# Kernel tuning notes

Measured on AMD Instinct MI355X. Metric: run time of the kernel, lower is better.

Reference implementation:

```python
import jax, jax.numpy as jnp
import numpy as np

INPUT_DIM, ENC_H, DEC_H, HORIZON = 8, 384, 384, 18
B, L = 1024, 336


def _lstm_layer(xs, Wih, Whh, bih, bhh):
    # xs: [B, L, D] -> outputs [B, L, H], final h [B, H]
    Bv = xs.shape[0]
    Hh = Whh.shape[1]
    def step(carry, x_t):
        h, c = carry
        z = x_t @ Wih.T + h @ Whh.T + bih + bhh  # [B, 4H], gate order i,f,g,o (PyTorch)
        i, f, g, o = jnp.split(z, 4, axis=-1)
        c = jax.nn.sigmoid(f) * c + jax.nn.sigmoid(i) * jnp.tanh(g)
        h = jax.nn.sigmoid(o) * jnp.tanh(c)
        return (h, c), h
    init = (jnp.zeros((Bv, Hh), xs.dtype), jnp.zeros((Bv, Hh), xs.dtype))
    (h, c), ys = jax.lax.scan(step, init, jnp.swapaxes(xs, 0, 1))
    return jnp.swapaxes(ys, 0, 1), h


def setup_inputs() -> dict:
    key = jax.random.key(0)
    ks = jax.random.split(key, 20)
    s = 0.05
    d = {
        "x": jax.random.normal(ks[0], (B, L, INPUT_DIM), jnp.float32),
        "future_feats": jax.random.normal(ks[1], (B, HORIZON, 4), jnp.float32),
        # encoder layer 0
        "enc_Wih0": jax.random.normal(ks[2], (4 * ENC_H, INPUT_DIM), jnp.float32) * s,
        "enc_Whh0": jax.random.normal(ks[3], (4 * ENC_H, ENC_H), jnp.float32) * s,
        "enc_bih0": jax.random.normal(ks[4], (4 * ENC_H,), jnp.float32) * s,
        "enc_bhh0": jax.random.normal(ks[5], (4 * ENC_H,), jnp.float32) * s,
        # encoder layer 1
        "enc_Wih1": jax.random.normal(ks[6], (4 * ENC_H, ENC_H), jnp.float32) * s,
        "enc_Whh1": jax.random.normal(ks[7], (4 * ENC_H, ENC_H), jnp.float32) * s,
        "enc_bih1": jax.random.normal(ks[8], (4 * ENC_H,), jnp.float32) * s,
        "enc_bhh1": jax.random.normal(ks[9], (4 * ENC_H,), jnp.float32) * s,
        # attention projection (no bias)
        "Wa": jax.random.normal(ks[10], (DEC_H, ENC_H), jnp.float32) * s,
        # dec_in: Linear(1+4+enc_h -> dec_h)
        "dec_in_W": jax.random.normal(ks[11], (DEC_H, 1 + 4 + ENC_H), jnp.float32) * s,
        "dec_in_b": jax.random.normal(ks[12], (DEC_H,), jnp.float32) * s,
        # decoder LSTM (1 layer)
        "dec_Wih": jax.random.normal(ks[13], (4 * DEC_H, DEC_H), jnp.float32) * s,
        "dec_Whh": jax.random.normal(ks[14], (4 * DEC_H, DEC_H), jnp.float32) * s,
        "dec_bih": jax.random.normal(ks[15], (4 * DEC_H,), jnp.float32) * s,
        "dec_bhh": jax.random.normal(ks[16], (4 * DEC_H,), jnp.float32) * s,
        # output head
        "out_W": jax.random.normal(ks[17], (1, DEC_H), jnp.float32) * s,
        "out_b": jax.random.normal(ks[18], (1,), jnp.float32) * s,
    }
    return d


def reference(x, future_feats, enc_Wih0, enc_Whh0, enc_bih0, enc_bhh0,
              enc_Wih1, enc_Whh1, enc_bih1, enc_bhh1, Wa, dec_in_W, dec_in_b,
              dec_Wih, dec_Whh, dec_bih, dec_bhh, out_W, out_b):
    Bv = x.shape[0]
    # 2-layer encoder (eval mode: inter-layer dropout inactive)
    h1, _ = _lstm_layer(x, enc_Wih0, enc_Whh0, enc_bih0, enc_bhh0)
    enc_out, h_last = _lstm_layer(h1, enc_Wih1, enc_Whh1, enc_bih1, enc_bhh1)
    proj = enc_out @ Wa.T  # [B, L, dec_h] (Wa(enc_out) is step-invariant)

    def dec_step(carry, feat_t):
        h, c, y_prev = carry
        scores = jnp.einsum('bld,bd->bl', proj, h)
        alpha = jax.nn.softmax(scores, axis=1)
        ctx = jnp.einsum('bl,bld->bd', alpha, enc_out)
        din = jnp.concatenate([y_prev, feat_t, ctx], axis=1)  # [B, 1+4+enc_h]
        din = jax.nn.relu(din @ dec_in_W.T + dec_in_b)
        z = din @ dec_Wih.T + h @ dec_Whh.T + dec_bih + dec_bhh
        i, f, g, o = jnp.split(z, 4, axis=-1)
        c = jax.nn.sigmoid(f) * c + jax.nn.sigmoid(i) * jnp.tanh(g)
        h = jax.nn.sigmoid(o) * jnp.tanh(c)
        y_t = h @ out_W.T + out_b  # [B, 1]
        y_prev = jax.lax.stop_gradient(y_t)  # .detach() in torch
        return (h, c, y_prev), y_t

    init = (h_last, jnp.zeros_like(h_last), jnp.zeros((Bv, 1), x.dtype))
    _, ys = jax.lax.scan(dec_step, init, jnp.swapaxes(future_feats, 0, 1))
    return jnp.swapaxes(ys, 0, 1)  # [B, horizon, 1]
```

## Files before the change

### kernel.cpp

```cpp
#include <hip/hip_runtime.h>
#include <stdint.h>

typedef __bf16 bf16;
typedef __bf16 bf16x8 __attribute__((ext_vector_type(8)));
typedef short  s16x8  __attribute__((ext_vector_type(8)));
typedef float  f32x4  __attribute__((ext_vector_type(4)));
typedef uint32_t u32;

#define NB   1024
#define LSEQ 336
#define HID  384
#define HOR  18
#define SMEM_BYTES 36864

__device__ bf16  g_H0[(size_t)(LSEQ+1)*NB*HID];
__device__ bf16  g_enc[(size_t)NB*LSEQ*HID];
__device__ bf16  g_zero[HID];
__device__ bf16  g_Adec[2*NB*768];
__device__ bf16  g_Adin[NB*416];
__device__ bf16  g_xb[NB*LSEQ*8];
__device__ float g_c0[NB*HID];
__device__ float g_c1[NB*HID];
__device__ float g_cdec[NB*HID];
__device__ float g_u[NB*HID];
__device__ float g_bias0[1536], g_bias1[1536], g_biasd[1536], g_biasdin[384];
__device__ bf16  g_Bp0[12*13*4096];
__device__ bf16  g_Bp1n[24*24*4*64*8];
__device__ bf16  g_Bpd[12*24*4096];
__device__ bf16  g_Bpi[3*13*4096];
__device__ bf16  g_Bpu[3*12*4096];
__device__ int   g_f0[8*LSEQ];
__device__ int   g_f1[4*(LSEQ+1)];

__device__ __forceinline__ float sigf(float x){ return 1.0f/(1.0f + __expf(-x)); }
__device__ __forceinline__ float tanh_f(float x){
  x = fminf(fmaxf(x, -15.f), 15.f);
  float e = __expf(2.f*x);
  return (e - 1.f)/(e + 1.f);
}

__device__ __forceinline__ void ds16(bf16* p, s16x8 v){
  union{ s16x8 v; uint64_t q[2]; } u; u.v = v;
  __hip_atomic_store((uint64_t*)p,     u.q[0], __ATOMIC_RELAXED, __HIP_MEMORY_SCOPE_AGENT);
  __hip_atomic_store((uint64_t*)p + 1, u.q[1], __ATOMIC_RELAXED, __HIP_MEMORY_SCOPE_AGENT);
}

__global__ void zero_state_k(){
  int i = blockIdx.x*blockDim.x + threadIdx.x;
  int st = gridDim.x*blockDim.x;
  bf16 z = (bf16)0.f;
  for(int k=i;k<NB*HID;k+=st){ g_H0[k]=z; g_c0[k]=0.f; g_c1[k]=0.f; g_cdec[k]=0.f; }
  for(int k=i;k<8*LSEQ;k+=st) g_f0[k]=0;
  for(int k=i;k<4*(LSEQ+1);k+=st) g_f1[k]=0;
}

__global__ void pack_xb_k(const float* __restrict__ x){
  int i = blockIdx.x*256 + threadIdx.x;
  int n = NB*LSEQ*8;
  for(int k=i; k<n; k+=gridDim.x*256) g_xb[k] = (bf16)x[k];
}

__global__ void pack_gates_k(int mode, const float* __restrict__ W1, const float* __restrict__ W2,
                             int nks){
  bf16* out = (mode==0)? g_Bp0 : g_Bpd;
  size_t idx = (size_t)blockIdx.x*256 + threadIdx.x;
  size_t total = (size_t)12*nks*512;
  if(idx >= total) return;
  int lane = (int)(idx & 63);
  int tt   = (int)((idx>>6) & 7);
  size_t tmp = idx >> 9;
  int ks = (int)(tmp % nks);
  int jb = (int)(tmp / nks);
  int n  = (tt>>1)*HID + jb*32 + (tt&1)*16 + (lane&15);
  int kb = ks*32 + (lane>>4)*8;
  bf16x8 v;
  #pragma unroll
  for(int i=0;i<8;i++){
    int k = kb + i;
    float f;
    if(mode==0) f = (k<384) ? W1[(size_t)n*384 + k] : (k<392 ? W2[(size_t)n*8 + (k-384)] : 0.f);
    else        f = (k<384) ? W1[(size_t)n*384 + k] : W2[(size_t)n*384 + (k-384)];
    v[i] = (bf16)f;
  }
  *(bf16x8*)(out + idx*8) = v;
}

__global__ void pack_gates16_k(const float* __restrict__ Wih1, const float* __restrict__ Whh1){
  int idx = blockIdx.x*256 + threadIdx.x;
  if(idx >= 24*24*4*64) return;
  int lane = idx&63, rem = idx>>6;
  int g = rem&3; rem >>= 2;
  int ks = rem%24, jn = rem/24;
  int n  = g*HID + jn*16 + (lane&15);
  int kb = ks*32 + (lane>>4)*8;
  bf16x8 v;
  #pragma unroll
  for(int i=0;i<8;i++){
    int k = kb+i;
    float f = (k<384)? Wih1[(size_t)n*384 + k] : Whh1[(size_t)n*384 + (k-384)];
    v[i] = (bf16)f;
  }
  *(bf16x8*)(g_Bp1n + (size_t)idx*8) = v;
}

__global__ void pack_plain_k(int mode, const float* __restrict__ W, int nks, int nb_cnt){
  bf16* out = mode ? g_Bpu : g_Bpi;
  size_t idx = (size_t)blockIdx.x*256 + threadIdx.x;
  size_t total = (size_t)nb_cnt*nks*512;
  if(idx>=total) return;
  int lane = (int)(idx&63);
  int tt   = (int)((idx>>6)&7);
  size_t tmp = idx>>9;
  int ks = (int)(tmp%nks);
  int nb = (int)(tmp/nks);
  int n  = nb*128 + tt*16 + (lane&15);
  int kb = ks*32 + (lane>>4)*8;
  bf16x8 v;
  #pragma unroll
  for(int i=0;i<8;i++){
    int k = kb+i;
    float f;
    if(mode==0) f = (k<389)? W[(size_t)n*389 + k] : 0.f;
    else        f = W[(size_t)k*384 + n];
    v[i]=(bf16)f;
  }
  *(bf16x8*)(out + idx*8) = v;
}

__global__ void prep_misc_k(const float* bih0,const float* bhh0,const float* bih1,const float* bhh1,
                            const float* dbih,const float* dbhh,const float* dinb){
  int i = blockIdx.x*256 + threadIdx.x;
  if(i<1536){ g_bias0[i]=bih0[i]+bhh0[i]; g_bias1[i]=bih1[i]+bhh1[i]; g_biasd[i]=dbih[i]+dbhh[i]; }
  if(i<384) g_biasdin[i]=dinb[i];
}

__device__ __forceinline__ void spin_ge(int* p, int tgt){
  while(__hip_atomic_load(p, __ATOMIC_RELAXED, __HIP_MEMORY_SCOPE_AGENT) < tgt)
    __builtin_amdgcn_s_sleep(1);
}

__global__ __launch_bounds__(256,1)
void enc6_k(){
  extern __shared__ char lds[];
  const int bid = blockIdx.x, tid = threadIdx.x;
  const int lane = tid&63, wv = tid>>6;
  const int l15 = lane&15, lk = (lane>>4)*8;

  if(bid < 96){
    const int g = bid & 7, jb = bid >> 3;
    { const s16x8* src = (const s16x8*)(g_Bp0 + (size_t)jb*13*4096);
      s16x8* dst = (s16x8*)lds;
      #pragma unroll
      for(int h=0;h<26;h++) dst[tid + h*256] = src[tid + h*256];
    }
    bf16* tr = (bf16*)(lds + 13*8192);
    __syncthreads();
    const int jj0 = jb*32 + l15;
    float bia[2],bfa[2],bga[2],boa[2];
    #pragma unroll
    for(int jh=0;jh<2;jh++){
      bia[jh]=g_bias0[jj0+jh*16];     bfa[jh]=g_bias0[384+jj0+jh*16];
      bga[jh]=g_bias0[768+jj0+jh*16]; boa[jh]=g_bias0[1152+jj0+jh*16];
    }
    size_t hoff[2], xoff[2];
    #pragma unroll
    for(int mt=0;mt<2;mt++){
      int row = g*128 + wv*32 + mt*16 + l15;
      hoff[mt] = (size_t)row*HID + lk;
      xoff[mt] = (size_t)row*LSEQ*8;
    }
    float c[2][2][4] = {};
    for(int w=0; w<LSEQ; w++){
      if(tid==0 && w>=1) spin_ge(&g_f0[g*LSEQ + (w-1)], 12);
      __syncthreads();
      asm volatile("" ::: "memory");
      const bf16* H0w = g_H0 + (size_t)w*NB*HID;
      bf16x8 af[13][2];
      #pragma unroll
      for(int ks=0;ks<12;ks++)
        #pragma unroll
        for(int mt=0;mt<2;mt++)
          af[ks][mt] = *(const bf16x8*)(H0w + hoff[mt] + ks*32);
      #pragma unroll
      for(int mt=0;mt<2;mt++){
        bf16x8 z;
        #pragma unroll
        for(int e=0;e<8;e++) z[e]=(bf16)0.f;
        if(lk==0) z = *(const bf16x8*)(g_xb + xoff[mt] + (size_t)w*8);
        af[12][mt] = z;
      }
      f32x4 acc[2][8];
      #pragma unroll
      for(int m2=0;m2<2;m2++)
        #pragma unroll
        for(int tt=0;tt<8;tt++) acc[m2][tt] = (f32x4){0.f,0.f,0.f,0.f};
      #pragma unroll
      for(int ks=0;ks<13;ks++){
        #pragma unroll
        for(int tt=0;tt<8;tt++){
          bf16x8 bfr = *(const bf16x8*)(lds + (ks*8+tt)*1024 + lane*16);
          acc[0][tt] = __builtin_amdgcn_mfma_f32_16x16x32_bf16(af[ks][0], bfr, acc[0][tt],0,0,0);
          acc[1][tt] = __builtin_amdgcn_mfma_f32_16x16x32_bf16(af[ks][1], bfr, acc[1][tt],0,0,0);
        }
      }
      #pragma unroll
      for(int mt=0;mt<2;mt++)
        #pragma unroll
        for(int jh=0;jh<2;jh++)
          #pragma unroll
          for(int r=0;r<4;r++){
            float zi=acc[mt][0+jh][r]+bia[jh], zf=acc[mt][2+jh][r]+bfa[jh],
                  zg=acc[mt][4+jh][r]+bga[jh], zo=acc[mt][6+jh][r]+boa[jh];
            size_t ci = (size_t)(g*128 + wv*32 + mt*16 + (lane>>4)*4 + r)*HID + jj0 + jh*16;
            float cn = sigf(zf)*g_c0[ci] + sigf(zi)*tanh_f(zg);
            g_c0[ci] = cn;
            int lr = wv*32 + mt*16 + (lane>>4)*4 + r;
            tr[lr*32 + jh*16 + l15] = (bf16)(sigf(zo)*tanh_f(cn));
          }
      __syncthreads();
      bf16* H0n = g_H0 + (size_t)(w+1)*NB*HID;
      #pragma unroll
      for(int h=0;h<2;h++){
        int p = tid + h*256;
        int row = p>>2, cc = p&3;
        s16x8 v = *(const s16x8*)(tr + row*32 + cc*8);
        ds16(H0n + (size_t)(g*128+row)*HID + jb*32 + cc*8, v);
      }
      __syncthreads();
      if(tid==0)
        __hip_atomic_fetch_add(&g_f0[g*LSEQ + w], 1, __ATOMIC_RELAXED, __HIP_MEMORY_SCOPE_AGENT);
    }
  } else {
    const int idx = bid-96, m = idx & 3, jn = idx >> 2;
    { const s16x8* src = (const s16x8*)(g_Bp1n + (size_t)jn*24*2048);
      s16x8* dst = (s16x8*)lds;
      #pragma unroll
      for(int h=0;h<24;h++) dst[tid + h*256] = src[tid + h*256];
    }
    bf16* tr = (bf16*)(lds + 24*4096);
    __syncthreads();
    const int jj = jn*16 + l15;
    const float bi=g_bias1[jj], bff=g_bias1[384+jj], bg=g_bias1[768+jj], bo=g_bias1[1152+jj];
    int rows[4]; size_t hoff[4];
    #pragma unroll
    for(int mt=0;mt<4;mt++){
      rows[mt] = m*256 + wv*64 + mt*16 + l15;
      hoff[mt] = (size_t)rows[mt]*HID + lk;
    }
    float c[4][4] = {};
    for(int s=1; s<=LSEQ; s++){
      if(tid==0){
        spin_ge(&g_f0[(2*m)*LSEQ + (s-1)], 12);
        spin_ge(&g_f0[(2*m+1)*LSEQ + (s-1)], 12);
        if(s>=2) spin_ge(&g_f1[m*(LSEQ+1) + (s-1)], 24);
      }
      __syncthreads();
      asm volatile("" ::: "memory");
      const bf16* H0s = g_H0 + (size_t)s*NB*HID;
      const size_t strideE = (s>=2)? (size_t)LSEQ*HID : 0;
      const bf16* Es = (s>=2)? (g_enc + (size_t)(s-2)*HID) : g_zero;
      size_t eoff[4];
      #pragma unroll
      for(int mt=0;mt<4;mt++) eoff[mt] = (size_t)rows[mt]*strideE + lk;
      bf16x8 ap[8][4];
      #pragma unroll
      for(int d=0; d<8; d++)
        #pragma unroll
        for(int mt=0;mt<4;mt++)
          ap[d][mt] = *(const bf16x8*)(H0s + hoff[mt] + d*32);
      f32x4 acc[4][4];
      #pragma unroll
      for(int mt=0;mt<4;mt++)
        #pragma unroll
        for(int g4=0;g4<4;g4++) acc[mt][g4] = (f32x4){0.f,0.f,0.f,0.f};
      #pragma unroll
      for(int ks=0;ks<24;ks++){
        bf16x8 bfr[4];
        #pragma unroll
        for(int g4=0;g4<4;g4++) bfr[g4] = *(const bf16x8*)(lds + (ks*4+g4)*1024 + lane*16);
        bf16x8 a[4];
        #pragma unroll
        for(int mt=0;mt<4;mt++) a[mt] = ap[ks&7][mt];
        int kn = ks+8;
        if(kn<24){
          if(kn<12){
            #pragma unroll
            for(int mt=0;mt<4;mt++) ap[ks&7][mt] = *(const bf16x8*)(H0s + hoff[mt] + kn*32);
          } else {
            #pragma unroll
            for(int mt=0;mt<4;mt++) ap[ks&7][mt] = *(const bf16x8*)(Es + eoff[mt] + (kn-12)*32);
          }
        }
        #pragma unroll
        for(int mt=0;mt<4;mt++)
          #pragma unroll
          for(int g4=0;g4<4;g4++)
            acc[mt][g4] = __builtin_amdgcn_mfma_f32_16x16x32_bf16(a[mt], bfr[g4], acc[mt][g4],0,0,0);
      }
      #pragma unroll
      for(int mt=0;mt<4;mt++)
        #pragma unroll
        for(int r=0;r<4;r++){
          float zi=acc[mt][0][r]+bi, zf=acc[mt][1][r]+bff,
                zg=acc[mt][2][r]+bg, zo=acc[mt][3][r]+bo;
          size_t ci = (size_t)(m*256 + wv*64 + mt*16 + (lane>>4)*4 + r)*HID + jj;
          float cn = sigf(zf)*g_c1[ci] + sigf(zi)*tanh_f(zg);
          g_c1[ci] = cn;
          int lr = wv*64 + mt*16 + (lane>>4)*4 + r;
          tr[lr*16 + l15] = (bf16)(sigf(zo)*tanh_f(cn));
        }
      __syncthreads();
      const int t = s-1;
      #pragma unroll
      for(int h=0;h<2;h++){
        int p = tid + h*256;
        int row = p>>1, hf2 = p&1;
        s16x8 v = *(const s16x8*)(tr + row*16 + hf2*8);
        ds16(g_enc + ((size_t)(m*256+row)*LSEQ + t)*HID + jn*16 + hf2*8, v);
      }
      __syncthreads();
      if(tid==0)
        __hip_atomic_fetch_add(&g_f1[m*(LSEQ+1) + s], 1, __ATOMIC_RELAXED, __HIP_MEMORY_SCOPE_AGENT);
    }
  }
}

struct SReg { s16x8 a0,a1,b0,b1; };

__device__ __forceinline__ void stage_load(const bf16* __restrict__ A, int ldA,
                                           const bf16* __restrict__ Bk, int tid, SReg& sr){
  int c0 = tid, c1 = tid+256;
  sr.a0 = *(const s16x8*)(A + (size_t)(c0>>2)*ldA + (c0&3)*8);
  sr.a1 = *(const s16x8*)(A + (size_t)(c1>>2)*ldA + (c1&3)*8);
  const s16x8* B8 = (const s16x8*)Bk;
  sr.b0 = B8[c0]; sr.b1 = B8[c1];
}

__device__ __forceinline__ void stage_write(char* Ab, char* Bb, int tid, const SReg& sr){
  int c0 = tid, c1 = tid+256;
  *(s16x8*)(Ab + (c0>>2)*80 + (c0&3)*16) = sr.a0;
  *(s16x8*)(Ab + (c1>>2)*80 + (c1&3)*16) = sr.a1;
  *(s16x8*)(Bb + c0*16) = sr.b0;
  *(s16x8*)(Bb + c1*16) = sr.b1;
}

__device__ __forceinline__ void gemm_core(const bf16* __restrict__ A, int ldA,
                                          const bf16* __restrict__ Bp, int nks,
                                          char* smem, f32x4 acc[4][4]){
  const int tid = threadIdx.x;
  const int lane = tid & 63, wv = tid>>6, wm = wv>>1, wn = wv&1;
  char* Ab0 = smem;            char* Ab1 = smem + 10240;
  char* Bb0 = smem + 20480;    char* Bb1 = smem + 28672;
  f32x4 z = {0.f,0.f,0.f,0.f};
  #pragma unroll
  for(int m=0;m<4;m++)
    #pragma unroll
    for(int g=0;g<4;g++) acc[m][g]=z;
  SReg sr;
  stage_load(A, ldA, Bp, tid, sr);
  stage_write(Ab0, Bb0, tid, sr);
  const int aoff = (wm*64 + (lane&15))*80 + (lane>>4)*16;
  const int boff = wn*1024 + lane*16;
  for(int ks=0; ks<nks; ks++){
    char* Ac = (ks&1)? Ab1: Ab0;
    char* Bc = (ks&1)? Bb1: Bb0;
    char* An = (ks&1)? Ab0: Ab1;
    char* Bn = (ks&1)? Bb0: Bb1;
    bool more = (ks+1)<nks;
    if(more) stage_load(A + (ks+1)*32, ldA, Bp + (size_t)(ks+1)*4096, tid, sr);
    __syncthreads();
    bf16x8 af[4], bfr[4];
    #pragma unroll
    for(int mt=0;mt<4;mt++) af[mt] = *(const bf16x8*)(Ac + aoff + mt*16*80);
    #pragma unroll
    for(int g=0;g<4;g++)    bfr[g] = *(const bf16x8*)(Bc + boff + g*2048);
    #pragma unroll
    for(int mt=0;mt<4;mt++)
      #pragma unroll
      for(int g=0;g<4;g++)
        acc[mt][g] = __builtin_amdgcn_mfma_f32_16x16x32_bf16(af[mt], bfr[g], acc[mt][g], 0,0,0);
    if(more) stage_write(An, Bn, tid, sr);
  }
}

__device__ __forceinline__ void lstm_epi(f32x4 acc[4][4], int mbase, int jb,
     const float* __restrict__ bias, float* __restrict__ cst,
     bf16* __restrict__ d0, int ld0, bf16* __restrict__ d1, size_t ld1){
  int lane = threadIdx.x&63, wv = threadIdx.x>>6, wm = wv>>1, wn = wv&1;
  int j = jb*32 + wn*16 + (lane&15);
  float bi = bias[j], bff = bias[384+j], bg = bias[768+j], bo = bias[1152+j];
  #pragma unroll
  for(int mt=0;mt<4;mt++){
    #pragma unroll
    for(int r=0;r<4;r++){
      int brow = mbase + wm*64 + mt*16 + (lane>>4)*4 + r;
      float zi = acc[mt][0][r]+bi, zf = acc[mt][1][r]+bff,
            zg = acc[mt][2][r]+bg, zo = acc[mt][3][r]+bo;
      size_t ci = (size_t)brow*HID + j;
      float cold = cst[ci];
      float cn = sigf(zf)*cold + sigf(zi)*tanh_f(zg);
      cst[ci] = cn;
      bf16 hb = (bf16)(sigf(zo)*tanh_f(cn));
      d0[(size_t)brow*ld0 + j] = hb;
      if(d1) d1[(size_t)brow*ld1 + j] = hb;
    }
  }
}

__global__ __launch_bounds__(256)
void dec_lstm_k(int t){
  __shared__ char smem[SMEM_BYTES];
  int bid = blockIdx.x, mb = bid/12, jb = bid%12;
  int rs = t&1, wsl = rs^1;
  f32x4 acc[4][4];
  gemm_core(g_Adec + (size_t)rs*NB*768 + (size_t)mb*128*768, 768,
            g_Bpd + (size_t)jb*24*4096, 24, smem, acc);
  lstm_epi(acc, mb*128, jb, g_biasd, g_cdec,
           g_Adec + (size_t)wsl*NB*768 + 384, 768, (bf16*)nullptr, 0);
}

__global__ __launch_bounds__(256)
void plain_gemm_k(int t, int mode){
  __shared__ char smem[SMEM_BYTES];
  int bid = blockIdx.x, mb = bid/3, nb = bid%3;
  int rs = t&1;
  const bf16* A; int ldA, nks; const bf16* Bp;
  if(mode==1){ A = g_Adec + (size_t)rs*NB*768 + 384; ldA=768; Bp = g_Bpu; nks=12; }
  else       { A = g_Adin;                           ldA=416; Bp = g_Bpi; nks=13; }
  f32x4 acc[4][4];
  gemm_core(A + (size_t)mb*128*ldA, ldA, Bp + (size_t)nb*nks*4096, nks, smem, acc);
  int lane = threadIdx.x&63, wv = threadIdx.x>>6, wm = wv>>1, wn = wv&1;
  bf16* dbf = g_Adec + (size_t)rs*NB*768;
  #pragma unroll
  for(int mt=0;mt<4;mt++){
    #pragma unroll
    for(int ti=0;ti<4;ti++){
      int n = nb*128 + (ti*2+wn)*16 + (lane&15);
      #pragma unroll
      for(int r=0;r<4;r++){
        int brow = mb*128 + wm*64 + mt*16 + (lane>>4)*4 + r;
        float v = acc[mt][ti][r];
        if(mode==0){ v += g_biasdin[n]; v = fmaxf(v,0.f); dbf[(size_t)brow*768 + n] = (bf16)v; }
        else g_u[(size_t)brow*384 + n] = v;
      }
    }
  }
}

__global__ __launch_bounds__(256)
void attn_k(){
  __shared__ float sm[4][392];
  int tid = threadIdx.x, lane = tid&63, w = tid>>6;
  int bl = w>>1, hf = w&1;
  int b = blockIdx.x*2 + bl;
  const float* ub = g_u + (size_t)b*HID + lane*6;
  float u0=ub[0],u1=ub[1],u2=ub[2],u3=ub[3],u4=ub[4],u5=ub[5];
  const u32* er = (const u32*)(g_enc + (size_t)b*LSEQ*HID) + (size_t)hf*168*192 + lane*3;
  float m=-1e30f, den=0.f, a0=0,a1=0,a2=0,a3=0,a4=0,a5=0;
  for(int l=0;l<168;l++){
    u32 w0 = er[0], w1 = er[1], w2 = er[2];
    er += 192;
    float e0 = __uint_as_float(w0<<16);
    float e1 = __uint_as_float(w0 & 0xffff0000u);
    float e2 = __uint_as_float(w1<<16);
    float e3 = __uint_as_float(w1 & 0xffff0000u);
    float e4 = __uint_as_float(w2<<16);
    float e5 = __uint_as_float(w2 & 0xffff0000u);
    float p = e0*u0 + e1*u1 + e2*u2 + e3*u3 + e4*u4 + e5*u5;
    #pragma unroll
    for(int o=1;o<64;o<<=1) p += __shfl_xor(p, o, 64);
    float mn = fmaxf(m, p);
    float al = __expf(m - mn), pe = __expf(p - mn);
    den = den*al + pe;
    a0 = a0*al + pe*e0; a1 = a1*al + pe*e1; a2 = a2*al + pe*e2;
    a3 = a3*al + pe*e3; a4 = a4*al + pe*e4; a5 = a5*al + pe*e5;
    m = mn;
  }
  if(lane==0){ sm[w][0]=m; sm[w][1]=den; }
  sm[w][2+lane*6+0]=a0; sm[w][2+lane*6+1]=a1; sm[w][2+lane*6+2]=a2;
  sm[w][2+lane*6+3]=a3; sm[w][2+lane*6+4]=a4; sm[w][2+lane*6+5]=a5;
  __syncthreads();
  if(hf==0){
    float m2 = sm[w+1][0], d2 = sm[w+1][1];
    float M = fmaxf(m, m2);
    float f1 = __expf(m - M), f2 = __expf(m2 - M);
    float inv = 1.f/(den*f1 + d2*f2);
    bf16* cd = g_Adin + (size_t)b*416 + 5 + lane*6;
    cd[0] = (bf16)((a0*f1 + sm[w+1][2+lane*6+0]*f2)*inv);
    cd[1] = (bf16)((a1*f1 + sm[w+1][2+lane*6+1]*f2)*inv);
    cd[2] = (bf16)((a2*f1 + sm[w+1][2+lane*6+2]*f2)*inv);
    cd[3] = (bf16)((a3*f1 + sm[w+1][2+lane*6+3]*f2)*inv);
    cd[4] = (bf16)((a4*f1 + sm[w+1][2+lane*6+4]*f2)*inv);
    cd[5] = (bf16)((a5*f1 + sm[w+1][2+lane*6+5]*f2)*inv);
  }
}

__global__ void post_k(int t, const float* __restrict__ outW,
                       const float* __restrict__ outb, float* __restrict__ out,
                       const float* __restrict__ ff){
  int b = blockIdx.x*256 + threadIdx.x;
  if(b>=NB) return;
  int wsl = (t&1)^1;
  const s16x8* hp = (const s16x8*)(g_Adec + (size_t)wsl*NB*768 + (size_t)b*768 + 384);
  float acc = 0.f;
  #pragma unroll 4
  for(int i=0;i<48;i++){
    s16x8 v = hp[i];
    #pragma unroll
    for(int e=0;e<8;e++){
      float hv = __uint_as_float(((u32)(uint16_t)v[e])<<16);
      acc += hv*outW[i*8+e];
    }
  }
  float y = acc + outb[0];
  out[(size_t)b*HOR + t] = y;
  g_Adin[(size_t)b*416] = (bf16)y;
  if(t+1<HOR){
    #pragma unroll
    for(int k=0;k<4;k++) g_Adin[(size_t)b*416 + 1 + k] = (bf16)ff[(size_t)b*HOR*4 + (t+1)*4 + k];
  }
}

__global__ void dec_prep_k(const float* __restrict__ ff){
  int i = blockIdx.x*256 + threadIdx.x;
  if(i < NB*HID){
    int b = i/HID, j = i%HID;
    g_Adec[(size_t)b*768 + 384 + j] = g_enc[(size_t)b*LSEQ*HID + (size_t)(LSEQ-1)*HID + j];
  }
  if(i < NB*4){
    int b = i>>2, k = i&3;
    g_Adin[(size_t)b*416 + 1 + k] = (bf16)ff[(size_t)b*HOR*4 + k];
  }
  if(i < NB) g_Adin[(size_t)i*416] = (bf16)0.f;
}

extern "C" void kernel_launch(void* const* d_in, const int* in_sizes, int n_in,
                              void* d_out, int out_size, void* d_ws, size_t ws_size,
                              hipStream_t stream){
  const float* x    = (const float*)d_in[0];
  const float* ff   = (const float*)d_in[1];
  const float* Wih0 = (const float*)d_in[2];
  const float* Whh0 = (const float*)d_in[3];
  const float* bih0 = (const float*)d_in[4];
  const float* bhh0 = (const float*)d_in[5];
  const float* Wih1 = (const float*)d_in[6];
  const float* Whh1 = (const float*)d_in[7];
  const float* bih1 = (const float*)d_in[8];
  const float* bhh1 = (const float*)d_in[9];
  const float* Wa   = (const float*)d_in[10];
  const float* dinW = (const float*)d_in[11];
  const float* dinb = (const float*)d_in[12];
  const float* dWih = (const float*)d_in[13];
  const float* dWhh = (const float*)d_in[14];
  const float* dbih = (const float*)d_in[15];
  const float* dbhh = (const float*)d_in[16];
  const float* outW = (const float*)d_in[17];
  const float* outb = (const float*)d_in[18];
  float* out = (float*)d_out;

  zero_state_k<<<1024,256,0,stream>>>();
  pack_xb_k<<<2048,256,0,stream>>>(x);
  pack_gates_k<<<(12*13*512)/256,256,0,stream>>>(0, Whh0, Wih0, 13);
  pack_gates16_k<<<576,256,0,stream>>>(Wih1, Whh1);
  pack_gates_k<<<(12*24*512)/256,256,0,stream>>>(2, dWih, dWhh, 24);
  pack_plain_k<<<(3*13*512)/256,256,0,stream>>>(0, dinW, 13, 3);
  pack_plain_k<<<(3*12*512)/256,256,0,stream>>>(1, Wa, 12, 3);
  prep_misc_k<<<8,256,0,stream>>>(bih0,bhh0,bih1,bhh1,dbih,dbhh,dinb);

  hipFuncSetAttribute((const void*)enc6_k,
                      hipFuncAttributeMaxDynamicSharedMemorySize, 114688);
  enc6_k<<<192,256,114688,stream>>>();

  dec_prep_k<<<1536,256,0,stream>>>(ff);
  for(int t=0;t<HOR;t++){
    plain_gemm_k<<<24,256,0,stream>>>(t, 1);
    attn_k<<<512,256,0,stream>>>();
    plain_gemm_k<<<24,256,0,stream>>>(t, 0);
    dec_lstm_k<<<96,256,0,stream>>>(t);
    post_k<<<4,256,0,stream>>>(t, outW, outb, out, ff);
  }
  (void)in_sizes; (void)n_in; (void)out_size; (void)d_ws; (void)ws_size;
}
```

Measured before the change: 8.753 ms.

## Keep encoder cell state in registers and fold output projection into next GEMM

Both encoder LSTM layers now carry the cell state in per-thread registers instead of reading and writing g_c0/g_c1 in global memory every timestep. This removes that global traffic and the zeroing of those buffers. The layer-1 blocks now split their three flag spin-waits across three threads so the waits run concurrently. In the decoder, the output projection and the writes of y_prev and the next step's features move into the next step's first plain_gemm launch, leaving a single post_k launch after the loop and cutting one launch per decoder step. This relies on each thread always owning the same (row, column) cell elements across timesteps, and it adds some register pressure in the persistent encoder kernel.

```diff
diff --git a/kernel.cpp b/kernel.cpp
--- a/kernel.cpp
+++ b/kernel.cpp
@@ -19,8 +19,6 @@
 __device__ bf16  g_Adec[2*NB*768];
 __device__ bf16  g_Adin[NB*416];
 __device__ bf16  g_xb[NB*LSEQ*8];
-__device__ float g_c0[NB*HID];
-__device__ float g_c1[NB*HID];
 __device__ float g_cdec[NB*HID];
 __device__ float g_u[NB*HID];
 __device__ float g_bias0[1536], g_bias1[1536], g_biasd[1536], g_biasdin[384];
@@ -49,7 +47,7 @@
   int i = blockIdx.x*blockDim.x + threadIdx.x;
   int st = gridDim.x*blockDim.x;
   bf16 z = (bf16)0.f;
-  for(int k=i;k<NB*HID;k+=st){ g_H0[k]=z; g_c0[k]=0.f; g_c1[k]=0.f; g_cdec[k]=0.f; }
+  for(int k=i;k<NB*HID;k+=st){ g_H0[k]=z; g_cdec[k]=0.f; }
   for(int k=i;k<8*LSEQ;k+=st) g_f0[k]=0;
   for(int k=i;k<4*(LSEQ+1);k+=st) g_f1[k]=0;
 }
@@ -140,7 +138,7 @@
 }
 
 __global__ __launch_bounds__(256,1)
-void enc6_k(){
+void enc7_k(){
   extern __shared__ char lds[];
   const int bid = blockIdx.x, tid = threadIdx.x;
   const int lane = tid&63, wv = tid>>6;
@@ -211,9 +209,8 @@
           for(int r=0;r<4;r++){
             float zi=acc[mt][0+jh][r]+bia[jh], zf=acc[mt][2+jh][r]+bfa[jh],
                   zg=acc[mt][4+jh][r]+bga[jh], zo=acc[mt][6+jh][r]+boa[jh];
-            size_t ci = (size_t)(g*128 + wv*32 + mt*16 + (lane>>4)*4 + r)*HID + jj0 + jh*16;
-            float cn = sigf(zf)*g_c0[ci] + sigf(zi)*tanh_f(zg);
-            g_c0[ci] = cn;
+            float cn = sigf(zf)*c[mt][jh][r] + sigf(zi)*tanh_f(zg);
+            c[mt][jh][r]=cn;
             int lr = wv*32 + mt*16 + (lane>>4)*4 + r;
             tr[lr*32 + jh*16 + l15] = (bf16)(sigf(zo)*tanh_f(cn));
           }
@@ -249,11 +246,9 @@
     }
     float c[4][4] = {};
     for(int s=1; s<=LSEQ; s++){
-      if(tid==0){
-        spin_ge(&g_f0[(2*m)*LSEQ + (s-1)], 12);
-        spin_ge(&g_f0[(2*m+1)*LSEQ + (s-1)], 12);
-        if(s>=2) spin_ge(&g_f1[m*(LSEQ+1) + (s-1)], 24);
-      }
+      if(tid==0)           spin_ge(&g_f0[(2*m)*LSEQ + (s-1)], 12);
+      else if(tid==1)      spin_ge(&g_f0[(2*m+1)*LSEQ + (s-1)], 12);
+      else if(tid==2 && s>=2) spin_ge(&g_f1[m*(LSEQ+1) + (s-1)], 24);
       __syncthreads();
       asm volatile("" ::: "memory");
       const bf16* H0s = g_H0 + (size_t)s*NB*HID;
@@ -303,9 +298,8 @@
         for(int r=0;r<4;r++){
           float zi=acc[mt][0][r]+bi, zf=acc[mt][1][r]+bff,
                 zg=acc[mt][2][r]+bg, zo=acc[mt][3][r]+bo;
-          size_t ci = (size_t)(m*256 + wv*64 + mt*16 + (lane>>4)*4 + r)*HID + jj;
-          float cn = sigf(zf)*g_c1[ci] + sigf(zi)*tanh_f(zg);
-          g_c1[ci] = cn;
+          float cn = sigf(zf)*c[mt][r] + sigf(zi)*tanh_f(zg);
+          c[mt][r]=cn;
           int lr = wv*64 + mt*16 + (lane>>4)*4 + r;
           tr[lr*16 + l15] = (bf16)(sigf(zo)*tanh_f(cn));
         }
@@ -420,7 +414,9 @@
 }
 
 __global__ __launch_bounds__(256)
-void plain_gemm_k(int t, int mode){
+void plain_gemm_k(int t, int mode, const float* __restrict__ outW,
+                  const float* __restrict__ outb, float* __restrict__ out,
+                  const float* __restrict__ ff){
   __shared__ char smem[SMEM_BYTES];
   int bid = blockIdx.x, mb = bid/3, nb = bid%3;
   int rs = t&1;
@@ -444,6 +440,25 @@
         else g_u[(size_t)brow*384 + n] = v;
       }
     }
+  }
+  if(mode==1 && t>=1 && nb==0 && threadIdx.x<128){
+    int b = mb*128 + threadIdx.x;
+    const s16x8* hp = (const s16x8*)(g_Adec + (size_t)rs*NB*768 + (size_t)b*768 + 384);
+    float acc2 = 0.f;
+    #pragma unroll 4
+    for(int i=0;i<48;i++){
+      s16x8 v = hp[i];
+      #pragma unroll
+      for(int e=0;e<8;e++){
+        float hv = __uint_as_float(((u32)(uint16_t)v[e])<<16);
+        acc2 += hv*outW[i*8+e];
+      }
+    }
+    float y = acc2 + outb[0];
+    out[(size_t)b*HOR + (t-1)] = y;
+    g_Adin[(size_t)b*416] = (bf16)y;
+    #pragma unroll
+    for(int k=0;k<4;k++) g_Adin[(size_t)b*416 + 1 + k] = (bf16)ff[(size_t)b*HOR*4 + t*4 + k];
   }
 }
 
@@ -496,8 +511,7 @@
 }
 
 __global__ void post_k(int t, const float* __restrict__ outW,
-                       const float* __restrict__ outb, float* __restrict__ out,
-                       const float* __restrict__ ff){
+                       const float* __restrict__ outb, float* __restrict__ out){
   int b = blockIdx.x*256 + threadIdx.x;
   if(b>=NB) return;
   int wsl = (t&1)^1;
@@ -512,13 +526,7 @@
       acc += hv*outW[i*8+e];
     }
   }
-  float y = acc + outb[0];
-  out[(size_t)b*HOR + t] = y;
-  g_Adin[(size_t)b*416] = (bf16)y;
-  if(t+1<HOR){
-    #pragma unroll
-    for(int k=0;k<4;k++) g_Adin[(size_t)b*416 + 1 + k] = (bf16)ff[(size_t)b*HOR*4 + (t+1)*4 + k];
-  }
+  out[(size_t)b*HOR + t] = acc + outb[0];
 }
 
 __global__ void dec_prep_k(const float* __restrict__ ff){
@@ -567,17 +575,17 @@
   pack_plain_k<<<(3*12*512)/256,256,0,stream>>>(1, Wa, 12, 3);
   prep_misc_k<<<8,256,0,stream>>>(bih0,bhh0,bih1,bhh1,dbih,dbhh,dinb);
 
-  hipFuncSetAttribute((const void*)enc6_k,
+  hipFuncSetAttribute((const void*)enc7_k,
                       hipFuncAttributeMaxDynamicSharedMemorySize, 114688);
-  enc6_k<<<192,256,114688,stream>>>();
+  enc7_k<<<192,256,114688,stream>>>();
 
   dec_prep_k<<<1536,256,0,stream>>>(ff);
   for(int t=0;t<HOR;t++){
-    plain_gemm_k<<<24,256,0,stream>>>(t, 1);
+    plain_gemm_k<<<24,256,0,stream>>>(t, 1, outW, outb, out, ff);
     attn_k<<<512,256,0,stream>>>();
-    plain_gemm_k<<<24,256,0,stream>>>(t, 0);
+    plain_gemm_k<<<24,256,0,stream>>>(t, 0, outW, outb, out, ff);
     dec_lstm_k<<<96,256,0,stream>>>(t);
-    post_k<<<4,256,0,stream>>>(t, outW, outb, out, ff);
-  }
+  }
+  post_k<<<4,256,0,stream>>>(17, outW, outb, out);
   (void)in_sizes; (void)n_in; (void)out_size; (void)d_ws; (void)ws_size;
 }
```

Result: faster. 8.571 ms (-2.1%).
